# Performance work log

Measured on AMD Instinct MI355X. Metric: run time of the kernel, lower is better.

## Reference

```python
import jax, jax.numpy as jnp
import numpy as np

EPS = 1e-5
SLOPE = 0.2
K = 20
B, N = 8, 2048

def _lrelu(x):
    return jnp.where(x >= 0, x, SLOPE * x)

def _bn(x, g, b, m, v, axis):
    # eval-mode batchnorm with running stats
    shape = [1] * x.ndim
    shape[axis] = -1
    g, b, m, v = (t.reshape(shape) for t in (g, b, m, v))
    return g * (x - m) * jax.lax.rsqrt(v + EPS) + b

def _knn(x, k):
    # x: (B, C, N) -> neighbor indices (B, N, k) by largest negative sq dist
    xx = jnp.sum(x * x, axis=1)                      # (B, N)
    inner = jnp.einsum('bcn,bcm->bnm', x, x)         # (B, N, N)
    pd = 2.0 * inner - xx[:, :, None] - xx[:, None, :]
    return jax.lax.top_k(pd, k)[1]

def _graph_feature(x, k):
    # x: (B, C, N) -> (B, 2C, N, k) edge features [nbr - center, center]
    idx = _knn(x, k)                                  # (B, N, k)
    xt = jnp.transpose(x, (0, 2, 1))                  # (B, N, C)
    nbr = xt[jnp.arange(x.shape[0])[:, None, None], idx]  # (B, N, k, C)
    center = xt[:, :, None, :]
    f = jnp.concatenate([nbr - center, jnp.broadcast_to(center, nbr.shape)], axis=-1)
    return jnp.transpose(f, (0, 3, 1, 2))

def _edge_block(x, W, g, b, m, v):
    f = _graph_feature(x, K)                          # (B, 2C, N, k)
    h = jnp.einsum('oc,bcnk->bonk', W, f)             # 1x1 conv
    return jnp.max(_lrelu(_bn(h, g, b, m, v, 1)), axis=-1)

def _forward(x, W1, bn1_g, bn1_b, bn1_m, bn1_v, W2, bn2_g, bn2_b, bn2_m, bn2_v, W3, bn3_g, bn3_b, bn3_m, bn3_v, W4, bn4_g, bn4_b, bn4_m, bn4_v, l1_w, l1_b, bn5_g, bn5_b, bn5_m, bn5_v, l2_w, l2_b, bn6_g, bn6_b, bn6_m, bn6_v, l3_w, l3_b):
    xc = jnp.transpose(x, (0, 2, 1))                  # (B, 3, N)
    x1 = _edge_block(xc, W1, bn1_g, bn1_b, bn1_m, bn1_v)   # (B, 64, N)
    x2 = _edge_block(x1, W2, bn2_g, bn2_b, bn2_m, bn2_v)   # (B, 64, N)
    x3 = _edge_block(x2, W3, bn3_g, bn3_b, bn3_m, bn3_v)   # (B, 128, N)
    h = jnp.concatenate([x1, x2, x3], axis=1)         # (B, 256, N)
    h = _lrelu(_bn(jnp.einsum('oc,bcn->bon', W4, h), bn4_g, bn4_b, bn4_m, bn4_v, 1))
    h = jnp.max(h, axis=-1)                           # (B, 1024)
    h = _lrelu(_bn(h @ l1_w.T + l1_b, bn5_g, bn5_b, bn5_m, bn5_v, 1))
    h = _lrelu(_bn(h @ l2_w.T + l2_b, bn6_g, bn6_b, bn6_m, bn6_v, 1))
    return h @ l3_w.T + l3_b                          # (B, 2)

def setup_inputs() -> dict:
    key = jax.random.key(0)
    ks = iter(jax.random.split(key, 64))
    def rn(shape, s=1.0):
        return jax.random.normal(next(ks), shape, jnp.float32) * s
    def add_bn(inp, prefix, c):
        inp[prefix + '_g'] = jax.random.uniform(next(ks), (c,), jnp.float32, 0.5, 1.5)
        inp[prefix + '_b'] = rn((c,), 0.1)
        inp[prefix + '_m'] = rn((c,), 0.1)
        inp[prefix + '_v'] = jax.random.uniform(next(ks), (c,), jnp.float32, 0.5, 1.5)
    inp = {'x': rn((B, N, 3))}
    inp['W1'] = rn((64, 6), 0.3); add_bn(inp, 'bn1', 64)
    inp['W2'] = rn((64, 128), 0.1); add_bn(inp, 'bn2', 64)
    inp['W3'] = rn((128, 128), 0.1); add_bn(inp, 'bn3', 128)
    inp['W4'] = rn((1024, 256), 0.08); add_bn(inp, 'bn4', 1024)
    inp['l1_w'] = rn((512, 1024), 0.03); inp['l1_b'] = rn((512,), 0.01); add_bn(inp, 'bn5', 512)
    inp['l2_w'] = rn((256, 512), 0.05); inp['l2_b'] = rn((256,), 0.01); add_bn(inp, 'bn6', 256)
    inp['l3_w'] = rn((2, 256), 0.06); inp['l3_b'] = rn((2,), 0.01)
    return inp

def reference(x, W1, bn1_g, bn1_b, bn1_m, bn1_v, W2, bn2_g, bn2_b, bn2_m, bn2_v, W3, bn3_g, bn3_b, bn3_m, bn3_v, W4, bn4_g, bn4_b, bn4_m, bn4_v, l1_w, l1_b, bn5_g, bn5_b, bn5_m, bn5_v, l2_w, l2_b, bn6_g, bn6_b, bn6_m, bn6_v, l3_w, l3_b):
    return _forward(x, W1, bn1_g, bn1_b, bn1_m, bn1_v, W2, bn2_g, bn2_b, bn2_m, bn2_v, W3, bn3_g, bn3_b, bn3_m, bn3_v, W4, bn4_g, bn4_b, bn4_m, bn4_v, l1_w, l1_b, bn5_g, bn5_b, bn5_m, bn5_v, l2_w, l2_b, bn6_g, bn6_b, bn6_m, bn6_v, l3_w, l3_b)
```

## Files before the change

### kernel.cpp

```cpp
#include <hip/hip_runtime.h>
#include <math.h>
#include <limits.h>

#define NN 2048
#define KK 20
#define EPSF 1e-5f

__device__ __forceinline__ float lrelu(float v){ return v >= 0.f ? v : 0.2f*v; }

__device__ __forceinline__ bool lexgt(float av, int ai, float bv, int bi){
  return (av > bv) || ((av == bv) && (ai < bi));
}

__device__ __forceinline__ void bsort64(float &v, int &id, int lane){
#pragma unroll
  for (int k = 2; k <= 64; k <<= 1){
#pragma unroll
    for (int j = k >> 1; j > 0; j >>= 1){
      float pv = __shfl_xor(v, j);
      int   pid = __shfl_xor(id, j);
      bool lower = (lane & j) == 0;
      bool desc  = (lane & k) == 0;
      bool mine_gt = lexgt(v, id, pv, pid);
      bool keep = (lower == desc) ? mine_gt : !mine_gt;
      v  = keep ? v  : pv;
      id = keep ? id : pid;
    }
  }
}

__device__ __forceinline__ void bmerge64(float &rv, int &rid, float nv, int nid, int lane){
  float xv  = __shfl(nv, 63 - lane);
  int   xid = __shfl(nid, 63 - lane);
  bool mine = lexgt(rv, rid, xv, xid);
  rv  = mine ? rv  : xv;
  rid = mine ? rid : xid;
#pragma unroll
  for (int j = 32; j > 0; j >>= 1){
    float pv = __shfl_xor(rv, j);
    int   pid = __shfl_xor(rid, j);
    bool lower = (lane & j) == 0;
    bool mine_gt = lexgt(rv, rid, pv, pid);
    bool keep = lower ? mine_gt : !mine_gt;
    rv  = keep ? rv  : pv;
    rid = keep ? rid : pid;
  }
}

__global__ void k_prep1(const float* __restrict__ x, const float* __restrict__ W1,
                        float* __restrict__ Y, float* __restrict__ T, float* __restrict__ SQ){
  __shared__ float wa[64][3], wd[64][3];
  int t = threadIdx.x;
  if (t < 64){
#pragma unroll
    for (int c=0;c<3;c++){
      float a = W1[t*6+c], b2 = W1[t*6+3+c];
      wa[t][c] = a; wd[t][c] = b2 - a;
    }
  }
  __syncthreads();
  int gid = blockIdx.x*256 + t;
  int b = gid >> 11, n = gid & (NN-1);
  float px = x[gid*3+0], py = x[gid*3+1], pz = x[gid*3+2];
  SQ[gid] = px*px + py*py + pz*pz;
  float* yb = Y + ((size_t)b*128)*NN + n;
  float* tb = T + ((size_t)b*128)*NN + n;
#pragma unroll 8
  for (int o=0;o<64;o++){
    yb[(size_t)o*NN] = wa[o][0]*px + wa[o][1]*py + wa[o][2]*pz;
    tb[(size_t)o*NN] = wd[o][0]*px + wd[o][1]*py + wd[o][2]*pz;
  }
}

__global__ __launch_bounds__(256) void k_knn3_bt(const float* __restrict__ x, const float* __restrict__ SQ,
                                                 int* __restrict__ IDX){
  __shared__ float cx[256], cy[256], cz[256], cq[256];
  int t = threadIdx.x;
  int lane = t & 63, w = t >> 6;
  int b = blockIdx.y;
  int n = blockIdx.x*4 + w;
  int gq = b*NN + n;
  float qx = x[gq*3], qy = x[gq*3+1], qz = x[gq*3+2];
  float qs = SQ[gq];
  float rv = -INFINITY; int rid = INT_MAX;
  for (int tile=0; tile<8; ++tile){
    __syncthreads();
    int m = tile*256 + t;
    int gm = b*NN + m;
    cx[t] = x[gm*3]; cy[t] = x[gm*3+1]; cz[t] = x[gm*3+2]; cq[t] = SQ[gm];
    __syncthreads();
#pragma unroll
    for (int sb=0; sb<4; ++sb){
      int ml = sb*64 + lane;
      float d = 2.f*(qx*cx[ml] + qy*cy[ml] + qz*cz[ml]) - qs - cq[ml];
      int idc = tile*256 + ml;
      float t20v = __shfl(rv, 19); int t20i = __shfl(rid, 19);
      if (__any(lexgt(d, idc, t20v, t20i))){
        bsort64(d, idc, lane);
        bmerge64(rv, rid, d, idc, lane);
      }
    }
  }
  if (lane < KK) IDX[((size_t)b*KK + lane)*NN + n] = rid;
}

__global__ void k_sqnorm(const float* __restrict__ X, float* __restrict__ SQ){
  int gid = blockIdx.x*256 + threadIdx.x;
  int b = gid >> 11, n = gid & (NN-1);
  const float* xb = X + (size_t)b*256*NN;
  float s = 0.f;
#pragma unroll
  for (int c=0;c<64;c++){ float vv = xb[(size_t)c*NN + n]; s += vv*vv; }
  SQ[gid] = s;
}

__global__ __launch_bounds__(256) void k_gram(const float* __restrict__ X, float* __restrict__ Dt, int mh){
  __shared__ __align__(16) float an[32][132];
  __shared__ __align__(16) float bm[32][132];
  int t = threadIdx.x;
  int io = t >> 4, in_ = t & 15;
  int mb = blockIdx.x * 128;
  int nb = blockIdx.y * 128;
  int b = blockIdx.z;
  const float* xb = X + (size_t)b*256*NN;
  int mg = mh*1024 + mb;
  float acc[8][8];
#pragma unroll
  for (int r=0;r<8;r++)
#pragma unroll
    for (int c=0;c<8;c++) acc[r][c]=0.f;
  for (int c0=0; c0<64; c0+=32){
    __syncthreads();
#pragma unroll
    for (int p=0;p<4;p++){
      int idx = p*256 + t;
      int cc = idx >> 5, n4 = (idx & 31) * 4;
      *(float4*)&an[cc][n4] = *(const float4*)&xb[(size_t)(c0+cc)*NN + nb + n4];
    }
#pragma unroll
    for (int p=0;p<4;p++){
      int idx = p*256 + t;
      int cc = idx >> 5, m4 = (idx & 31) * 4;
      *(float4*)&bm[cc][m4] = *(const float4*)&xb[(size_t)(c0+cc)*NN + mg + m4];
    }
    __syncthreads();
#pragma unroll 4
    for (int c=0;c<32;c++){
      float4 a0 = *(const float4*)&an[c][io*8];
      float4 a1 = *(const float4*)&an[c][io*8+4];
      float4 b0 = *(const float4*)&bm[c][in_*8];
      float4 b1 = *(const float4*)&bm[c][in_*8+4];
      float ar[8] = {a0.x,a0.y,a0.z,a0.w,a1.x,a1.y,a1.z,a1.w};
      float br[8] = {b0.x,b0.y,b0.z,b0.w,b1.x,b1.y,b1.z,b1.w};
#pragma unroll
      for (int r=0;r<8;r++)
#pragma unroll
        for (int s=0;s<8;s++) acc[r][s] += ar[r]*br[s];
    }
  }
#pragma unroll
  for (int r=0;r<8;r++){
    size_t row = ((size_t)b*NN + nb + io*8 + r)*1024 + mb + in_*8;
    *(float4*)&Dt[row]   = make_float4(acc[r][0],acc[r][1],acc[r][2],acc[r][3]);
    *(float4*)&Dt[row+4] = make_float4(acc[r][4],acc[r][5],acc[r][6],acc[r][7]);
  }
}

__global__ __launch_bounds__(256) void k_sel_bt(const float* __restrict__ Dt, const float* __restrict__ SQ,
                                                int mh, int phase,
                                                float* __restrict__ RV, int* __restrict__ RI,
                                                int* __restrict__ IDX){
  int t = threadIdx.x;
  int lane = t & 63, w = t >> 6;
  int b = blockIdx.y;
  int n = blockIdx.x*4 + w;
  float qs = SQ[b*NN + n];
  float rv; int rid;
  if (phase == 0){ rv = -INFINITY; rid = INT_MAX; }
  else {
    if (lane < KK){ rv = RV[((size_t)b*NN + n)*KK + lane]; rid = RI[((size_t)b*NN + n)*KK + lane]; }
    else          { rv = -INFINITY; rid = INT_MAX; }
  }
  const float* drow = Dt + ((size_t)b*NN + n)*1024;
  const float* sqh  = SQ + b*NN + mh*1024;
#pragma unroll
  for (int sb=0; sb<16; ++sb){
    int ml = sb*64 + lane;
    float d = 2.f*drow[ml] - qs - sqh[ml];
    int idc = mh*1024 + ml;
    float t20v = __shfl(rv, 19); int t20i = __shfl(rid, 19);
    if (__any(lexgt(d, idc, t20v, t20i))){
      bsort64(d, idc, lane);
      bmerge64(rv, rid, d, idc, lane);
    }
  }
  if (phase == 0){
    if (lane < KK){
      RV[((size_t)b*NN + n)*KK + lane] = rv;
      RI[((size_t)b*NN + n)*KK + lane] = rid;
    }
  } else {
    if (lane < KK) IDX[((size_t)b*KK + lane)*NN + n] = rid;
  }
}

__global__ __launch_bounds__(256) void k_edge_apply(const float* __restrict__ Y, const float* __restrict__ T,
                             const int* __restrict__ IDX,
                             const float* __restrict__ g, const float* __restrict__ be,
                             const float* __restrict__ mu, const float* __restrict__ va,
                             float* __restrict__ OUT, int c_off){
  int t = threadIdx.x;
  int nl = t & 127, oh = t >> 7;
  int n = blockIdx.x*128 + nl;
  int b = blockIdx.z;
  int o0 = blockIdx.y*32 + oh*16;
  int idx[KK];
#pragma unroll
  for (int k2=0;k2<KK;k2++) idx[k2] = IDX[((size_t)b*KK + k2)*NN + n];
  for (int oo=0;oo<16;oo++){
    int o = o0 + oo;
    const float* yrow = Y + ((size_t)b*128 + o)*NN;
    float M = -INFINITY;
#pragma unroll
    for (int k2=0;k2<KK;k2++) M = fmaxf(M, yrow[idx[k2]]);
    float s = g[o] * rsqrtf(va[o] + EPSF);
    float val = s*(M + T[((size_t)b*128 + o)*NN + n] - mu[o]) + be[o];
    OUT[((size_t)b*256 + c_off + o)*NN + n] = lrelu(val);
  }
}

template<int O>
__global__ __launch_bounds__(256) void k_yt_gemm(const float* __restrict__ X, const float* __restrict__ W,
                                                 float* __restrict__ Y, float* __restrict__ T){
  __shared__ __align__(16) float wa[O][64];
  __shared__ __align__(16) float wd[O][64];
  int t = threadIdx.x;
  for (int i=t; i<O*64; i+=256){
    int o = i >> 6, c = i & 63;
    float a = W[o*128 + c];
    wa[o][c] = a;
    wd[o][c] = W[o*128 + 64 + c] - a;
  }
  __syncthreads();
  int half = t >> 7, ln = t & 127;
  int gid = blockIdx.x*128 + ln;
  int b = gid >> 11, n = gid & (NN-1);
  const float* xb = X + (size_t)b*256*NN;
  float q[64];
#pragma unroll
  for (int c=0;c<64;c++) q[c] = xb[(size_t)c*NN + n];
  int o0 = half * (O/2);
  for (int o=o0; o<o0+O/2; ++o){
    float ay=0.f, at=0.f;
#pragma unroll
    for (int c=0;c<64;c+=4){
      float4 a4 = *(const float4*)&wa[o][c];
      float4 d4 = *(const float4*)&wd[o][c];
      ay += a4.x*q[c] + a4.y*q[c+1] + a4.z*q[c+2] + a4.w*q[c+3];
      at += d4.x*q[c] + d4.y*q[c+1] + d4.z*q[c+2] + d4.w*q[c+3];
    }
    Y[((size_t)b*128 + o)*NN + n] = ay;
    T[((size_t)b*128 + o)*NN + n] = at;
  }
}

__global__ __launch_bounds__(256) void k_w4t(const float* __restrict__ W4, float* __restrict__ W4T){
  __shared__ float Tt[64][65];
  int t = threadIdx.x;
  int c0 = blockIdx.x * 64, o0 = blockIdx.y * 64;
#pragma unroll
  for (int p=0;p<16;p++){
    int f = p*256 + t;
    int i = f >> 6, j = f & 63;
    Tt[i][j] = W4[(size_t)(o0+i)*256 + c0 + j];
  }
  __syncthreads();
#pragma unroll
  for (int p=0;p<16;p++){
    int f = p*256 + t;
    int i = f >> 6, j = f & 63;
    W4T[(size_t)(c0+i)*1024 + o0 + j] = Tt[j][i];
  }
}

__global__ __launch_bounds__(256) void k_w4max(const float* __restrict__ CAT, const float* __restrict__ W4T,
                                               float* __restrict__ PART){
  __shared__ __align__(16) float wt[32][132];
  __shared__ __align__(16) float ct[32][132];
  int t = threadIdx.x;
  int io = t >> 4, in_ = t & 15;
  int nb = blockIdx.x * 128, ob = blockIdx.y * 128, b = blockIdx.z;
  const float* catb = CAT + (size_t)b*256*NN;
  float acc[8][8];
#pragma unroll
  for (int r=0;r<8;r++)
#pragma unroll
    for (int c=0;c<8;c++) acc[r][c]=0.f;
  for (int c0=0; c0<256; c0+=32){
    __syncthreads();
#pragma unroll
    for (int p=0;p<4;p++){
      int idx = p*256 + t;
      int cc = idx >> 5, o4 = (idx & 31) * 4;
      *(float4*)&wt[cc][o4] = *(const float4*)&W4T[(size_t)(c0+cc)*1024 + ob + o4];
    }
#pragma unroll
    for (int p=0;p<4;p++){
      int idx = p*256 + t;
      int cc = idx >> 5, n4 = (idx & 31) * 4;
      *(float4*)&ct[cc][n4] = *(const float4*)&catb[(size_t)(c0+cc)*NN + nb + n4];
    }
    __syncthreads();
#pragma unroll 4
    for (int c=0;c<32;c++){
      float4 a0 = *(const float4*)&wt[c][io*8];
      float4 a1 = *(const float4*)&wt[c][io*8+4];
      float4 b0 = *(const float4*)&ct[c][in_*8];
      float4 b1 = *(const float4*)&ct[c][in_*8+4];
      float ar[8] = {a0.x,a0.y,a0.z,a0.w,a1.x,a1.y,a1.z,a1.w};
      float br[8] = {b0.x,b0.y,b0.z,b0.w,b1.x,b1.y,b1.z,b1.w};
#pragma unroll
      for (int r=0;r<8;r++)
#pragma unroll
        for (int s=0;s<8;s++) acc[r][s] += ar[r]*br[s];
    }
  }
#pragma unroll
  for (int r=0;r<8;r++){
    float m = acc[r][0];
#pragma unroll
    for (int s=1;s<8;s++) m = fmaxf(m, acc[r][s]);
    m = fmaxf(m, __shfl_xor(m, 1));
    m = fmaxf(m, __shfl_xor(m, 2));
    m = fmaxf(m, __shfl_xor(m, 4));
    m = fmaxf(m, __shfl_xor(m, 8));
    if (in_ == 0){
      int o = ob + io*8 + r;
      PART[((size_t)b*1024 + o)*16 + blockIdx.x] = m;
    }
  }
}

__global__ void k_reduce4(const float* __restrict__ PART,
                          const float* __restrict__ g, const float* __restrict__ be,
                          const float* __restrict__ mu, const float* __restrict__ va,
                          float* __restrict__ H4){
  int gid = blockIdx.x*256 + threadIdx.x;
  int o = gid & 1023;
  float M = -INFINITY;
#pragma unroll
  for (int i=0;i<16;i++) M = fmaxf(M, PART[(size_t)gid*16 + i]);
  float s = g[o]*rsqrtf(va[o]+EPSF);
  H4[gid] = lrelu(s*(M - mu[o]) + be[o]);
}

__global__ __launch_bounds__(256) void k_mlp(const float* __restrict__ H4,
      const float* __restrict__ l1w, const float* __restrict__ l1b,
      const float* __restrict__ g5, const float* __restrict__ b5,
      const float* __restrict__ m5, const float* __restrict__ v5,
      const float* __restrict__ l2w, const float* __restrict__ l2b,
      const float* __restrict__ g6, const float* __restrict__ b6,
      const float* __restrict__ m6, const float* __restrict__ v6,
      const float* __restrict__ l3w, const float* __restrict__ l3b,
      float* __restrict__ out){
  __shared__ float h[1024];
  __shared__ float h5[512];
  __shared__ float h6[256];
  int b = blockIdx.x, t = threadIdx.x;
  for (int i=t;i<1024;i+=256) h[i] = H4[b*1024+i];
  __syncthreads();
  for (int o=t;o<512;o+=256){
    float acc = l1b[o];
    for (int c=0;c<1024;c+=4){
      float4 w = *(const float4*)&l1w[(size_t)o*1024 + c];
      acc += w.x*h[c] + w.y*h[c+1] + w.z*h[c+2] + w.w*h[c+3];
    }
    float s = g5[o]*rsqrtf(v5[o]+EPSF);
    h5[o] = lrelu(s*(acc - m5[o]) + b5[o]);
  }
  __syncthreads();
  if (t < 256){
    int o = t;
    float acc = l2b[o];
    for (int c=0;c<512;c+=4){
      float4 w = *(const float4*)&l2w[(size_t)o*512 + c];
      acc += w.x*h5[c] + w.y*h5[c+1] + w.z*h5[c+2] + w.w*h5[c+3];
    }
    float s = g6[o]*rsqrtf(v6[o]+EPSF);
    h6[o] = lrelu(s*(acc - m6[o]) + b6[o]);
  }
  __syncthreads();
  if (t < 128){
    int o = t >> 6, l = t & 63;
    float p = 0.f;
#pragma unroll
    for (int j=0;j<4;j++){ int c = j*64 + l; p += l3w[o*256 + c]*h6[c]; }
    p += __shfl_xor(p, 32); p += __shfl_xor(p, 16); p += __shfl_xor(p, 8);
    p += __shfl_xor(p, 4);  p += __shfl_xor(p, 2);  p += __shfl_xor(p, 1);
    if (l == 0) out[b*2 + o] = p + l3b[o];
  }
}

extern "C" void kernel_launch(void* const* d_in, const int* in_sizes, int n_in,
                              void* d_out, int out_size, void* d_ws, size_t ws_size,
                              hipStream_t stream){
  (void)in_sizes; (void)n_in; (void)out_size; (void)ws_size;
  const float* x    = (const float*)d_in[0];
  const float* W1   = (const float*)d_in[1];
  const float* bn1g = (const float*)d_in[2];
  const float* bn1b = (const float*)d_in[3];
  const float* bn1m = (const float*)d_in[4];
  const float* bn1v = (const float*)d_in[5];
  const float* W2   = (const float*)d_in[6];
  const float* bn2g = (const float*)d_in[7];
  const float* bn2b = (const float*)d_in[8];
  const float* bn2m = (const float*)d_in[9];
  const float* bn2v = (const float*)d_in[10];
  const float* W3   = (const float*)d_in[11];
  const float* bn3g = (const float*)d_in[12];
  const float* bn3b = (const float*)d_in[13];
  const float* bn3m = (const float*)d_in[14];
  const float* bn3v = (const float*)d_in[15];
  const float* W4   = (const float*)d_in[16];
  const float* bn4g = (const float*)d_in[17];
  const float* bn4b = (const float*)d_in[18];
  const float* bn4m = (const float*)d_in[19];
  const float* bn4v = (const float*)d_in[20];
  const float* l1w  = (const float*)d_in[21];
  const float* l1b  = (const float*)d_in[22];
  const float* bn5g = (const float*)d_in[23];
  const float* bn5b = (const float*)d_in[24];
  const float* bn5m = (const float*)d_in[25];
  const float* bn5v = (const float*)d_in[26];
  const float* l2w  = (const float*)d_in[27];
  const float* l2b  = (const float*)d_in[28];
  const float* bn6g = (const float*)d_in[29];
  const float* bn6b = (const float*)d_in[30];
  const float* bn6m = (const float*)d_in[31];
  const float* bn6v = (const float*)d_in[32];
  const float* l3w  = (const float*)d_in[33];
  const float* l3b  = (const float*)d_in[34];

  float* CAT  = (float*)d_ws;
  float* Yb   = CAT + (size_t)8*256*NN;
  float* Tb   = Yb  + (size_t)8*128*NN;
  float* SQ   = Tb  + (size_t)8*128*NN;
  int*   IDX  = (int*)(SQ + (size_t)8*NN);
  float* PART = (float*)(IDX + (size_t)8*KK*NN);
  float* H4   = PART + (size_t)8*1024*16;
  float* W4T  = H4 + (size_t)8*1024;
  float* RV   = W4T + (size_t)256*1024;
  int*   RI   = (int*)(RV + (size_t)8*NN*KK);
  float* Dt   = (float*)(RI + (size_t)8*NN*KK);

  k_w4t<<<dim3(4,16),256,0,stream>>>(W4, W4T);
  k_prep1<<<64,256,0,stream>>>(x, W1, Yb, Tb, SQ);
  k_knn3_bt<<<dim3(512,8),256,0,stream>>>(x, SQ, IDX);
  k_edge_apply<<<dim3(16,2,8),256,0,stream>>>(Yb, Tb, IDX, bn1g, bn1b, bn1m, bn1v, CAT, 0);
  k_sqnorm<<<64,256,0,stream>>>(CAT, SQ);
  k_gram<<<dim3(8,16,8),256,0,stream>>>(CAT, Dt, 0);
  k_sel_bt<<<dim3(512,8),256,0,stream>>>(Dt, SQ, 0, 0, RV, RI, IDX);
  k_gram<<<dim3(8,16,8),256,0,stream>>>(CAT, Dt, 1);
  k_sel_bt<<<dim3(512,8),256,0,stream>>>(Dt, SQ, 1, 1, RV, RI, IDX);
  k_yt_gemm<64><<<128,256,0,stream>>>(CAT, W2, Yb, Tb);
  k_edge_apply<<<dim3(16,2,8),256,0,stream>>>(Yb, Tb, IDX, bn2g, bn2b, bn2m, bn2v, CAT, 64);
  k_sqnorm<<<64,256,0,stream>>>(CAT + (size_t)64*NN, SQ);
  k_gram<<<dim3(8,16,8),256,0,stream>>>(CAT + (size_t)64*NN, Dt, 0);
  k_sel_bt<<<dim3(512,8),256,0,stream>>>(Dt, SQ, 0, 0, RV, RI, IDX);
  k_gram<<<dim3(8,16,8),256,0,stream>>>(CAT + (size_t)64*NN, Dt, 1);
  k_sel_bt<<<dim3(512,8),256,0,stream>>>(Dt, SQ, 1, 1, RV, RI, IDX);
  k_yt_gemm<128><<<128,256,0,stream>>>(CAT + (size_t)64*NN, W3, Yb, Tb);
  k_edge_apply<<<dim3(16,4,8),256,0,stream>>>(Yb, Tb, IDX, bn3g, bn3b, bn3m, bn3v, CAT, 128);
  k_w4max<<<dim3(16,8,8),256,0,stream>>>(CAT, W4T, PART);
  k_reduce4<<<32,256,0,stream>>>(PART, bn4g, bn4b, bn4m, bn4v, H4);
  k_mlp<<<8,256,0,stream>>>(H4, l1w, l1b, bn5g, bn5b, bn5m, bn5v,
                            l2w, l2b, bn6g, bn6b, bn6m, bn6v, l3w, l3b, (float*)d_out);
}
```

Measured before the change: 1.429 ms.

## Replace wave bitonic kNN on 3D points with per-thread insertion lists plus merge

```diff
diff --git a/kernel.cpp b/kernel.cpp
--- a/kernel.cpp
+++ b/kernel.cpp
@@ -72,36 +72,87 @@
   }
 }
 
-__global__ __launch_bounds__(256) void k_knn3_bt(const float* __restrict__ x, const float* __restrict__ SQ,
-                                                 int* __restrict__ IDX){
-  __shared__ float cx[256], cy[256], cz[256], cq[256];
-  int t = threadIdx.x;
-  int lane = t & 63, w = t >> 6;
+__global__ __launch_bounds__(256) void k_knn3_part(const float* __restrict__ x, const float* __restrict__ SQ,
+                                                   float* __restrict__ PV, unsigned short* __restrict__ PI){
+  __shared__ __align__(16) float cd[128*4];
+  int t = threadIdx.x;
+  int half = blockIdx.x & 1, nb = blockIdx.x >> 1;
   int b = blockIdx.y;
-  int n = blockIdx.x*4 + w;
+  int n_base = nb * 32;
+  int cbase = half * 1024;
+  int ql = t & 31, sp = t >> 5;
+  int n = n_base + ql;
   int gq = b*NN + n;
   float qx = x[gq*3], qy = x[gq*3+1], qz = x[gq*3+2];
   float qs = SQ[gq];
-  float rv = -INFINITY; int rid = INT_MAX;
+  float v[KK]; int id[KK];
+#pragma unroll
+  for (int i=0;i<KK;i++){ v[i] = -INFINITY; id[i] = 0; }
+  int mlo = sp * 16;
   for (int tile=0; tile<8; ++tile){
+    int m0 = cbase + tile * 128;
     __syncthreads();
-    int m = tile*256 + t;
-    int gm = b*NN + m;
-    cx[t] = x[gm*3]; cy[t] = x[gm*3+1]; cz[t] = x[gm*3+2]; cq[t] = SQ[gm];
+#pragma unroll
+    for (int i=0;i<2;i++){
+      int f2 = t + i*256;
+      int m = f2 >> 2, ch = f2 & 3;
+      int gm = b*NN + m0 + m;
+      cd[f2] = (ch < 3) ? x[gm*3 + ch] : SQ[gm];
+    }
     __syncthreads();
-#pragma unroll
-    for (int sb=0; sb<4; ++sb){
-      int ml = sb*64 + lane;
-      float d = 2.f*(qx*cx[ml] + qy*cy[ml] + qz*cz[ml]) - qs - cq[ml];
-      int idc = tile*256 + ml;
-      float t20v = __shfl(rv, 19); int t20i = __shfl(rid, 19);
-      if (__any(lexgt(d, idc, t20v, t20i))){
-        bsort64(d, idc, lane);
-        bmerge64(rv, rid, d, idc, lane);
+    for (int j=mlo; j<mlo+16; ++j){
+      float4 c4 = *(const float4*)&cd[j*4];
+      float d = 2.f*(qx*c4.x + qy*c4.y + qz*c4.z) - qs - c4.w;
+      if (d > v[KK-1]){
+#pragma unroll
+        for (int jj = KK-1; jj >= 1; --jj){
+          bool cjm1 = d > v[jj-1];
+          bool cj   = d > v[jj];
+          float nv = cjm1 ? v[jj-1] : (cj ? d : v[jj]);
+          int   ni = cjm1 ? id[jj-1] : (cj ? (m0+j) : id[jj]);
+          v[jj] = nv; id[jj] = ni;
+        }
+        if (d > v[0]) { v[0] = d; id[0] = m0 + j; }
       }
     }
   }
-  if (lane < KK) IDX[((size_t)b*KK + lane)*NN + n] = rid;
+  size_t base = ((size_t)b*16 + half*8 + sp)*KK;
+#pragma unroll
+  for (int r=0;r<KK;r++){
+    PV[(base + r)*NN + n] = v[r];
+    PI[(base + r)*NN + n] = (unsigned short)id[r];
+  }
+}
+
+__global__ void k_topk_merge16(const float* __restrict__ PV, const unsigned short* __restrict__ PI,
+                               int* __restrict__ IDX){
+  int gid = blockIdx.x*256 + threadIdx.x;
+  int b = gid >> 11, n = gid & (NN-1);
+  float hv[16]; int hi_[16]; int hp[16];
+#pragma unroll
+  for (int s=0;s<16;s++){
+    hp[s] = 0;
+    hv[s] = PV[(((size_t)b*16 + s)*KK)*NN + n];
+    hi_[s] = (int)PI[(((size_t)b*16 + s)*KK)*NN + n];
+  }
+  for (int r=0;r<KK;r++){
+    float bv = hv[0]; int bi = hi_[0]; int bs = 0;
+#pragma unroll
+    for (int s=1;s<16;s++){
+      bool win = (hv[s] > bv) || ((hv[s] == bv) && (hi_[s] < bi));
+      bv = win ? hv[s] : bv; bi = win ? hi_[s] : bi; bs = win ? s : bs;
+    }
+    IDX[((size_t)b*KK + r)*NN + n] = bi;
+#pragma unroll
+    for (int s=0;s<16;s++){
+      if (s == bs){
+        int np = hp[s] + 1; hp[s] = np;
+        bool ok = np < KK;
+        hv[s]  = ok ? PV[(((size_t)b*16 + s)*KK + np)*NN + n] : -INFINITY;
+        hi_[s] = ok ? (int)PI[(((size_t)b*16 + s)*KK + np)*NN + n] : 0x7FFFFFFF;
+      }
+    }
+  }
 }
 
 __global__ void k_sqnorm(const float* __restrict__ X, float* __restrict__ SQ){
@@ -173,34 +224,47 @@
   int t = threadIdx.x;
   int lane = t & 63, w = t >> 6;
   int b = blockIdx.y;
-  int n = blockIdx.x*4 + w;
-  float qs = SQ[b*NN + n];
-  float rv; int rid;
-  if (phase == 0){ rv = -INFINITY; rid = INT_MAX; }
+  int n0 = blockIdx.x*8 + w*2;
+  int n1 = n0 + 1;
+  float qs0 = SQ[b*NN + n0], qs1 = SQ[b*NN + n1];
+  float rv0, rv1; int rid0, rid1;
+  if (phase == 0){ rv0 = rv1 = -INFINITY; rid0 = rid1 = INT_MAX; }
   else {
-    if (lane < KK){ rv = RV[((size_t)b*NN + n)*KK + lane]; rid = RI[((size_t)b*NN + n)*KK + lane]; }
-    else          { rv = -INFINITY; rid = INT_MAX; }
-  }
-  const float* drow = Dt + ((size_t)b*NN + n)*1024;
+    if (lane < KK){
+      rv0 = RV[((size_t)b*NN + n0)*KK + lane]; rid0 = RI[((size_t)b*NN + n0)*KK + lane];
+      rv1 = RV[((size_t)b*NN + n1)*KK + lane]; rid1 = RI[((size_t)b*NN + n1)*KK + lane];
+    } else { rv0 = rv1 = -INFINITY; rid0 = rid1 = INT_MAX; }
+  }
+  const float* drow0 = Dt + ((size_t)b*NN + n0)*1024;
+  const float* drow1 = drow0 + 1024;
   const float* sqh  = SQ + b*NN + mh*1024;
 #pragma unroll
   for (int sb=0; sb<16; ++sb){
     int ml = sb*64 + lane;
-    float d = 2.f*drow[ml] - qs - sqh[ml];
-    int idc = mh*1024 + ml;
-    float t20v = __shfl(rv, 19); int t20i = __shfl(rid, 19);
-    if (__any(lexgt(d, idc, t20v, t20i))){
-      bsort64(d, idc, lane);
-      bmerge64(rv, rid, d, idc, lane);
+    float sqm = sqh[ml];
+    float d0 = 2.f*drow0[ml] - qs0 - sqm;
+    float d1 = 2.f*drow1[ml] - qs1 - sqm;
+    int idc0 = mh*1024 + ml, idc1 = idc0;
+    float t0v = __shfl(rv0, 19); int t0i = __shfl(rid0, 19);
+    float t1v = __shfl(rv1, 19); int t1i = __shfl(rid1, 19);
+    bool trig = __any(lexgt(d0, idc0, t0v, t0i)) || __any(lexgt(d1, idc1, t1v, t1i));
+    if (trig){
+      bsort64(d0, idc0, lane);
+      bsort64(d1, idc1, lane);
+      bmerge64(rv0, rid0, d0, idc0, lane);
+      bmerge64(rv1, rid1, d1, idc1, lane);
     }
   }
   if (phase == 0){
     if (lane < KK){
-      RV[((size_t)b*NN + n)*KK + lane] = rv;
-      RI[((size_t)b*NN + n)*KK + lane] = rid;
+      RV[((size_t)b*NN + n0)*KK + lane] = rv0; RI[((size_t)b*NN + n0)*KK + lane] = rid0;
+      RV[((size_t)b*NN + n1)*KK + lane] = rv1; RI[((size_t)b*NN + n1)*KK + lane] = rid1;
     }
   } else {
-    if (lane < KK) IDX[((size_t)b*KK + lane)*NN + n] = rid;
+    if (lane < KK){
+      IDX[((size_t)b*KK + lane)*NN + n0] = rid0;
+      IDX[((size_t)b*KK + lane)*NN + n1] = rid1;
+    }
   }
 }
 
@@ -452,23 +516,26 @@
   float* RV   = W4T + (size_t)256*1024;
   int*   RI   = (int*)(RV + (size_t)8*NN*KK);
   float* Dt   = (float*)(RI + (size_t)8*NN*KK);
+  float* PTV  = Dt;
+  unsigned short* PTI = (unsigned short*)(PTV + (size_t)8*16*KK*NN);
 
   k_w4t<<<dim3(4,16),256,0,stream>>>(W4, W4T);
   k_prep1<<<64,256,0,stream>>>(x, W1, Yb, Tb, SQ);
-  k_knn3_bt<<<dim3(512,8),256,0,stream>>>(x, SQ, IDX);
+  k_knn3_part<<<dim3(128,8),256,0,stream>>>(x, SQ, PTV, PTI);
+  k_topk_merge16<<<64,256,0,stream>>>(PTV, PTI, IDX);
   k_edge_apply<<<dim3(16,2,8),256,0,stream>>>(Yb, Tb, IDX, bn1g, bn1b, bn1m, bn1v, CAT, 0);
   k_sqnorm<<<64,256,0,stream>>>(CAT, SQ);
   k_gram<<<dim3(8,16,8),256,0,stream>>>(CAT, Dt, 0);
-  k_sel_bt<<<dim3(512,8),256,0,stream>>>(Dt, SQ, 0, 0, RV, RI, IDX);
+  k_sel_bt<<<dim3(256,8),256,0,stream>>>(Dt, SQ, 0, 0, RV, RI, IDX);
   k_gram<<<dim3(8,16,8),256,0,stream>>>(CAT, Dt, 1);
-  k_sel_bt<<<dim3(512,8),256,0,stream>>>(Dt, SQ, 1, 1, RV, RI, IDX);
+  k_sel_bt<<<dim3(256,8),256,0,stream>>>(Dt, SQ, 1, 1, RV, RI, IDX);
   k_yt_gemm<64><<<128,256,0,stream>>>(CAT, W2, Yb, Tb);
   k_edge_apply<<<dim3(16,2,8),256,0,stream>>>(Yb, Tb, IDX, bn2g, bn2b, bn2m, bn2v, CAT, 64);
   k_sqnorm<<<64,256,0,stream>>>(CAT + (size_t)64*NN, SQ);
   k_gram<<<dim3(8,16,8),256,0,stream>>>(CAT + (size_t)64*NN, Dt, 0);
-  k_sel_bt<<<dim3(512,8),256,0,stream>>>(Dt, SQ, 0, 0, RV, RI, IDX);
+  k_sel_bt<<<dim3(256,8),256,0,stream>>>(Dt, SQ, 0, 0, RV, RI, IDX);
   k_gram<<<dim3(8,16,8),256,0,stream>>>(CAT + (size_t)64*NN, Dt, 1);
-  k_sel_bt<<<dim3(512,8),256,0,stream>>>(Dt, SQ, 1, 1, RV, RI, IDX);
+  k_sel_bt<<<dim3(256,8),256,0,stream>>>(Dt, SQ, 1, 1, RV, RI, IDX);
   k_yt_gemm<128><<<128,256,0,stream>>>(CAT + (size_t)64*NN, W3, Yb, Tb);
   k_edge_apply<<<dim3(16,4,8),256,0,stream>>>(Yb, Tb, IDX, bn3g, bn3b, bn3m, bn3v, CAT, 128);
   k_w4max<<<dim3(16,8,8),256,0,stream>>>(CAT, W4T, PART);
```

After: 1.520 ms. +6.4%, slower.
